# Kernel tuning notes

Hardware: AMD Instinct MI355X
Metric: run time of the kernel (lower is better)

The kernel has to match this reference:

```python
import jax, jax.numpy as jnp
import numpy as np

B, NA, NMAX, NC = 32, 8400, 32, 80
TOPK, ALPHA, BETA, EPS, BG_IDX = 13, 1.0, 6.0, 1e-9, 80
IMG = 640.0


def _ciou(box1, box2, eps=1e-7):
    # box1: (b, nmax, 1, 4) xyxy, box2: (b, 1, na, 4) xyxy -> CIoU (b, nmax, na)
    b1_x1, b1_y1, b1_x2, b1_y2 = (box1[..., 0], box1[..., 1], box1[..., 2], box1[..., 3])
    b2_x1, b2_y1, b2_x2, b2_y2 = (box2[..., 0], box2[..., 1], box2[..., 2], box2[..., 3])
    inter = (jnp.minimum(b1_x2, b2_x2) - jnp.maximum(b1_x1, b2_x1)).clip(0) * \
            (jnp.minimum(b1_y2, b2_y2) - jnp.maximum(b1_y1, b2_y1)).clip(0)
    w1, h1 = b1_x2 - b1_x1, b1_y2 - b1_y1 + eps
    w2, h2 = b2_x2 - b2_x1, b2_y2 - b2_y1 + eps
    union = w1 * h1 + w2 * h2 - inter + eps
    iou = inter / union
    cw = jnp.maximum(b1_x2, b2_x2) - jnp.minimum(b1_x1, b2_x1)
    ch = jnp.maximum(b1_y2, b2_y2) - jnp.minimum(b1_y1, b2_y1)
    c2 = cw * cw + ch * ch + eps
    rho2 = ((b2_x1 + b2_x2 - b1_x1 - b1_x2) ** 2 + (b2_y1 + b2_y2 - b1_y1 - b1_y2) ** 2) / 4.0
    v = (4.0 / np.pi ** 2) * (jnp.arctan(w2 / h2) - jnp.arctan(w1 / h1)) ** 2
    alpha = jax.lax.stop_gradient(v / (v - iou + (1.0 + eps)))
    return iou - (rho2 / c2 + v * alpha)


def _rand_boxes(key, shape):
    # well-formed xyxy boxes inside a 640x640 image
    k1, k2 = jax.random.split(key)
    xy = jax.random.uniform(k1, shape[:-1] + (2,), jnp.float32) * (IMG - 64.0)
    wh = jax.random.uniform(k2, shape[:-1] + (2,), jnp.float32) * 56.0 + 8.0
    return jnp.concatenate([xy, xy + wh], axis=-1)


def setup_inputs() -> dict:
    key = jax.random.key(0)
    ks = jax.random.split(key, 6)
    pd_scores = jax.random.uniform(ks[0], (B, NA, NC), jnp.float32)
    pd_bboxes = _rand_boxes(ks[1], (B, NA, 4))
    anc_points = jax.random.uniform(ks[2], (NA, 2), jnp.float32) * IMG
    gt_labels = jax.random.randint(ks[3], (B, NMAX, 1), 0, NC, dtype=jnp.int32)
    gt_bboxes = _rand_boxes(ks[4], (B, NMAX, 4))
    mask_gt = jnp.ones((B, NMAX, 1), jnp.float32)
    return {"pd_scores": pd_scores, "pd_bboxes": pd_bboxes, "anc_points": anc_points,
            "gt_labels": gt_labels, "gt_bboxes": gt_bboxes, "mask_gt": mask_gt}


def reference(pd_scores, pd_bboxes, anc_points, gt_labels, gt_bboxes, mask_gt):
    b, na, nc = pd_scores.shape
    nmax = gt_bboxes.shape[1]
    # pairwise CIoU between every GT and every predicted box: (b, nmax, na)
    overlaps = _ciou(gt_bboxes[:, :, None, :], pd_bboxes[:, None, :, :])
    # gather predicted class score at each GT's label: (b, nmax, na)
    p = jnp.transpose(pd_scores, (0, 2, 1))                     # (b, nc, na)
    scores = jnp.take_along_axis(p, gt_labels.astype(jnp.int32), axis=1)
    align_metric = (scores ** ALPHA) * (overlaps ** BETA)
    # top-k anchors per GT along the anchor axis, scatter to a boolean mask
    _, topk_idx = jax.lax.top_k(align_metric, TOPK)             # (b, nmax, topk)
    bi = jnp.arange(b)[:, None, None]
    gi = jnp.arange(nmax)[None, :, None]
    mask_pos = jnp.zeros((b, nmax, na), bool).at[bi, gi, topk_idx].set(True)
    target_gt_idx = jnp.argmax(mask_pos, axis=1)                # (b, na)
    fg_mask = mask_pos.sum(axis=1) > 0                          # (b, na)
    # gather assigned GT label / box per anchor
    target_labels = jnp.take_along_axis(gt_labels[..., 0].astype(jnp.int32), target_gt_idx, axis=1)
    target_bboxes = jnp.take_along_axis(gt_bboxes, target_gt_idx[..., None], axis=1)  # (b, na, 4)
    target_scores = jax.nn.one_hot(target_labels, nc, dtype=jnp.float32) * fg_mask[..., None]
    target_labels = jnp.where(fg_mask, target_labels, BG_IDX)
    # normalize target scores by mean positive overlap per anchor, clamped to [0, 1]
    mpf = mask_pos.astype(overlaps.dtype)
    pos_overlaps = jnp.clip((overlaps * mpf).sum(axis=1) / (mpf.sum(axis=1) + EPS), 0.0, 1.0)
    target_scores = target_scores * pos_overlaps[..., None]
    return target_labels, target_bboxes, target_scores, fg_mask, target_gt_idx
```

## Files before the change

### kernel.cpp

```cpp
#include <hip/hip_runtime.h>
#include <math.h>

#define BATCH 32
#define NA 8400
#define NMAX 32
#define NC 80
#define TOPK 13
#define THREADS 256
#define NF4ROW (NA / 4)
#define NPT4 9
#define TILE 128
#define NTILES 66
#define SSTRIDE 81

#define OFF_BOX 268800
#define OFF_SCR 1344000
#define OFF_FG  22848000
#define OFF_TGT 23116800
#define SCR_ELEMS (OFF_FG - OFF_SCR)
#define SCR_F4    (SCR_ELEMS / 4)
#define ZPB_M     2546

typedef float f32x4 __attribute__((ext_vector_type(4)));

__device__ __forceinline__ float ciou_f(float gx1, float gy1, float gx2, float gy2,
                                        float px1, float py1, float px2, float py2) {
    const float eps = 1e-7f;
    float iw = fmaxf(fminf(gx2, px2) - fmaxf(gx1, px1), 0.0f);
    float ih = fmaxf(fminf(gy2, py2) - fmaxf(gy1, py1), 0.0f);
    float inter = iw * ih;
    float w1 = gx2 - gx1, h1 = gy2 - gy1 + eps;
    float w2 = px2 - px1, h2 = py2 - py1 + eps;
    float uni = w1 * h1 + w2 * h2 - inter + eps;
    float iou = inter / uni;
    float cw = fmaxf(gx2, px2) - fminf(gx1, px1);
    float ch = fmaxf(gy2, py2) - fminf(gy1, py1);
    float c2 = cw * cw + ch * ch + eps;
    float dx = px1 + px2 - gx1 - gx2;
    float dy = py1 + py2 - gy1 - gy2;
    float rho2 = (dx * dx + dy * dy) / 4.0f;
    float dd = atanf(w2 / h2) - atanf(w1 / h1);
    float v = (float)(4.0 / (M_PI * M_PI)) * dd * dd;
    float alpha = v / (v - iou + (1.0f + eps));
    return iou - (rho2 / c2 + v * alpha);
}

__global__ __launch_bounds__(THREADS, 3) void metric_kernel(
    const float* __restrict__ pd_scores, const float* __restrict__ pd_bboxes,
    const int* __restrict__ gt_labels, const float* __restrict__ gt_bboxes,
    float* __restrict__ met, unsigned int* __restrict__ mask,
    float* __restrict__ zbase) {
    const int b = blockIdx.y;
    const int abase = blockIdx.x * TILE;
    const int tid = threadIdx.x;
    const int na_tile = min(TILE, NA - abase);
    const float eps = 1e-7f;

    if (tid < na_tile) mask[(size_t)b * NA + abase + tid] = 0u;

    __shared__ float ssc[TILE][SSTRIDE];
    __shared__ float4 spbox[TILE];
    __shared__ float sgx1[NMAX], sgy1[NMAX], sgx2[NMAX], sgy2[NMAX];
    __shared__ float sa1[NMAX], sat1[NMAX];
    __shared__ int   slbl[NMAX];

    if (tid < NMAX) {
        float4 g = ((const float4*)gt_bboxes)[b * NMAX + tid];
        float w1 = g.z - g.x, h1 = g.w - g.y + eps;
        sgx1[tid] = g.x; sgy1[tid] = g.y; sgx2[tid] = g.z; sgy2[tid] = g.w;
        sa1[tid]  = w1 * h1;
        sat1[tid] = atanf(w1 / h1);
        slbl[tid] = gt_labels[b * NMAX + tid];
    } else if (tid >= 128) {
        int al = tid - 128;
        if (al < na_tile)
            spbox[al] = ((const float4*)pd_bboxes)[(size_t)b * NA + abase + al];
    }

    const f32x4* srec4 = (const f32x4*)(pd_scores + ((size_t)b * NA + abase) * NC);
    const int nf4 = na_tile * 20;
    f32x4 r[10];
#pragma unroll
    for (int i = 0; i < 10; i++) {
        int f = tid + i * THREADS;
        if (f < nf4) r[i] = __builtin_nontemporal_load(srec4 + f);
    }
#pragma unroll
    for (int i = 0; i < 10; i++) {
        int f = tid + i * THREADS;
        if (f < nf4) {
            int a = f / 20, c = f % 20;
            float* d = &ssc[a][c * 4];
            d[0] = r[i][0]; d[1] = r[i][1]; d[2] = r[i][2]; d[3] = r[i][3];
        }
    }
    __syncthreads();

    if (zbase) {
        const int bid = b * NTILES + blockIdx.x;
        const size_t zoff = (size_t)bid * ZPB_M;
        f32x4* zp = (f32x4*)zbase + zoff;
        const f32x4 z = { 0.f, 0.f, 0.f, 0.f };
#pragma unroll
        for (int i = 0; i < 10; i++) {
            int j = tid + i * THREADS;
            if (j < ZPB_M && zoff + j < SCR_F4)
                __builtin_nontemporal_store(z, zp + j);
        }
    }

    const int al = tid & (TILE - 1);
    const int gbase = (tid >> 7) * 16;
    if (al >= na_tile) return;

    float4 p = spbox[al];
    float w2 = p.z - p.x, h2 = p.w - p.y + eps;
    float a2  = w2 * h2;
    float at2 = atanf(w2 / h2);
    const size_t abs_a = (size_t)abase + al;

#pragma unroll
    for (int k = 0; k < 16; k++) {
        int gi = gbase + k;
        float gx1 = sgx1[gi], gy1 = sgy1[gi], gx2 = sgx2[gi], gy2 = sgy2[gi];
        float iw = fmaxf(fminf(gx2, p.z) - fmaxf(gx1, p.x), 0.0f);
        float ih = fmaxf(fminf(gy2, p.w) - fmaxf(gy1, p.y), 0.0f);
        float inter = iw * ih;
        float uni = sa1[gi] + a2 - inter + eps;
        float iou = inter / uni;
        float cw = fmaxf(gx2, p.z) - fminf(gx1, p.x);
        float ch = fmaxf(gy2, p.w) - fminf(gy1, p.y);
        float c2 = cw * cw + ch * ch + eps;
        float dx = p.x + p.z - gx1 - gx2;
        float dy = p.y + p.w - gy1 - gy2;
        float rho2 = (dx * dx + dy * dy) / 4.0f;
        float dd = at2 - sat1[gi];
        float v = (float)(4.0 / (M_PI * M_PI)) * dd * dd;
        float alpha = v / (v - iou + (1.0f + eps));
        float ov = iou - (rho2 / c2 + v * alpha);
        float sc = ssc[al][slbl[gi]];
        float ov2 = ov * ov;
        met[((size_t)b * NMAX + gi) * NA + abs_a] = sc * (ov2 * ov2 * ov2);
    }
}

__global__ __launch_bounds__(THREADS) void topk_kernel(
    const float* __restrict__ met, unsigned int* __restrict__ mask) {
    const int tid  = threadIdx.x;
    const int lane = tid & 63;
    const int w    = tid >> 6;
    const int bid  = blockIdx.x;
    const int b  = bid >> 5;
    const int gi = bid & 31;
    const f32x4* mrow4 = (const f32x4*)(met + ((size_t)b * NMAX + gi) * NA);

    f32x4 m4[NPT4];
#pragma unroll
    for (int j = 0; j < NPT4; j++) {
        int f = j * THREADS + tid;
        if (f < NF4ROW) m4[j] = mrow4[f];
    }

    float bv0 = -INFINITY, bv1 = -INFINITY;
    int   ba0 = 0x7FFFFFFF, ba1 = 0x7FFFFFFF;
#pragma unroll
    for (int j = 0; j < NPT4; j++) {
        int f = j * THREADS + tid;
        bool vf = (f < NF4ROW);
#pragma unroll
        for (int c = 0; c < 4; c++) {
            float v = vf ? m4[j][c] : -INFINITY;
            int   a = vf ? 4 * f + c : 0x7FFFFFFF;
            bool beats0 = (v > bv0) || (v == bv0 && a < ba0);
            bool beats1 = (v > bv1) || (v == bv1 && a < ba1);
            if (beats0) { bv1 = bv0; ba1 = ba0; bv0 = v; ba0 = a; }
            else if (beats1) { bv1 = v; ba1 = a; }
        }
    }
    bool valid1 = true;

    float rv = -INFINITY; int ra = 0x7FFFFFFF;
    for (int k = 0; k < TOPK; k++) {
        float v = bv0; int a = ba0;
#pragma unroll
        for (int s = 1; s < 64; s <<= 1) {
            float ov = __shfl_xor(v, s);
            int   oa = __shfl_xor(a, s);
            if (ov > v || (ov == v && oa < a)) { v = ov; a = oa; }
        }
        if (lane == k) { rv = v; ra = a; }
        if (ba0 == a) {
            if (valid1) { bv0 = bv1; ba0 = ba1; valid1 = false; }
            else {
                float nv = -INFINITY; int na_ = 0x7FFFFFFF;
#pragma unroll
                for (int j = 0; j < NPT4; j++) {
                    int f = j * THREADS + tid;
                    bool vf = (f < NF4ROW);
#pragma unroll
                    for (int c = 0; c < 4; c++) {
                        float mv = vf ? m4[j][c] : -INFINITY;
                        int   ma = vf ? 4 * f + c : 0x7FFFFFFF;
                        bool below = (mv < v) || (mv == v && ma > a);
                        bool beats = (mv > nv) || (mv == nv && ma < na_);
                        if (below && beats && vf) { nv = mv; na_ = ma; }
                    }
                }
                bv0 = nv; ba0 = na_;
            }
        }
    }

    __shared__ float lv[4 * TOPK];
    __shared__ int   la[4 * TOPK];
    if (lane < TOPK) { lv[w * TOPK + lane] = rv; la[w * TOPK + lane] = ra; }
    __syncthreads();

    if (w == 0) {
        float v = (lane < 4 * TOPK) ? lv[lane] : -INFINITY;
        int   a = (lane < 4 * TOPK) ? la[lane] : 0x7FFFFFFF;
        for (int k = 0; k < TOPK; k++) {
            float wv = v; int wa = a;
#pragma unroll
            for (int s = 1; s < 64; s <<= 1) {
                float ov = __shfl_xor(wv, s);
                int   oa = __shfl_xor(wa, s);
                if (ov > wv || (ov == wv && oa < wa)) { wv = ov; wa = oa; }
            }
            if (lane == 0) atomicOr(&mask[(size_t)b * NA + wa], 1u << gi);
            if (a == wa) { v = -INFINITY; a = 0x7FFFFFFF; }
        }
    }
}

__global__ __launch_bounds__(THREADS) void zero_scr_kernel(float* __restrict__ out) {
    f32x4* p = (f32x4*)(out + OFF_SCR);
    const f32x4 z = { 0.f, 0.f, 0.f, 0.f };
    const int stride = gridDim.x * THREADS;
    for (int i = blockIdx.x * THREADS + threadIdx.x; i < SCR_F4; i += stride)
        __builtin_nontemporal_store(z, p + i);
}

__global__ __launch_bounds__(THREADS) void assign_kernel(
    const float* __restrict__ pd_bboxes, const int* __restrict__ gt_labels,
    const float* __restrict__ gt_bboxes, const unsigned int* __restrict__ mask,
    float* __restrict__ out) {
    const int idx = blockIdx.x * THREADS + threadIdx.x;
    const int b = idx / NA;

    unsigned msk = mask[idx];
    int tgt = msk ? (__ffs(msk) - 1) : 0;
    float4 gb = ((const float4*)gt_bboxes)[b * NMAX + tgt];
    int lbl = gt_labels[b * NMAX + tgt];
    float4 p = ((const float4*)pd_bboxes)[idx];

    float sum = 0.0f;
    int cnt = 0;
    unsigned mm = msk;
    while (mm) {
        int i = __ffs(mm) - 1;
        mm &= mm - 1;
        float4 g = ((const float4*)gt_bboxes)[b * NMAX + i];
        sum += ciou_f(g.x, g.y, g.z, g.w, p.x, p.y, p.z, p.w);
        cnt++;
    }
    float po = fminf(fmaxf(sum / ((float)cnt + 1e-9f), 0.0f), 1.0f);

    bool fg = (msk != 0);
    __builtin_nontemporal_store(fg ? (float)lbl : 80.0f, &out[idx]);
    f32x4 gbv = { gb.x, gb.y, gb.z, gb.w };
    __builtin_nontemporal_store(gbv, (f32x4*)(out + OFF_BOX) + idx);
    __builtin_nontemporal_store(fg ? 1.0f : 0.0f, &out[OFF_FG + idx]);
    __builtin_nontemporal_store((float)tgt, &out[OFF_TGT + idx]);
    if (fg) out[OFF_SCR + (size_t)idx * NC + lbl] = po;
}

extern "C" void kernel_launch(void* const* d_in, const int* in_sizes, int n_in,
                              void* d_out, int out_size, void* d_ws, size_t ws_size,
                              hipStream_t stream) {
    const float* pd_scores = (const float*)d_in[0];
    const float* pd_bboxes = (const float*)d_in[1];
    const int*   gt_labels = (const int*)d_in[3];
    const float* gt_bboxes = (const float*)d_in[4];

    float* out = (float*)d_out;
    unsigned int* mask = (unsigned int*)d_ws;

    const size_t MASK_BYTES = (size_t)BATCH * NA * 4;
    const size_t MET_BYTES  = (size_t)BATCH * NMAX * NA * 4;
    const size_t met_off = (MASK_BYTES + 255) & ~(size_t)255;
    const bool ws_met = (ws_size >= met_off + MET_BYTES);

    float* met = ws_met ? (float*)((char*)d_ws + met_off) : out + OFF_SCR;

    dim3 g1(NTILES, BATCH);
    if (ws_met) {
        metric_kernel<<<g1, THREADS, 0, stream>>>(pd_scores, pd_bboxes,
                                                  gt_labels, gt_bboxes, met, mask,
                                                  out + OFF_SCR);
        topk_kernel<<<BATCH * NMAX, THREADS, 0, stream>>>(met, mask);
    } else {
        metric_kernel<<<g1, THREADS, 0, stream>>>(pd_scores, pd_bboxes,
                                                  gt_labels, gt_bboxes, met, mask,
                                                  nullptr);
        topk_kernel<<<BATCH * NMAX, THREADS, 0, stream>>>(met, mask);
        zero_scr_kernel<<<2048, THREADS, 0, stream>>>(out);
    }
    assign_kernel<<<BATCH * NA / THREADS, THREADS, 0, stream>>>(
        pd_bboxes, gt_labels, gt_bboxes, mask, out);
}
```

Baseline: 86.81 us.

## Compact score tile to per-GT columns and raise metric kernel occupancy

The metric kernel no longer stores the full 80-class score row per anchor in shared memory. It builds a class-to-GT bitmask and scatters only the score columns used by the 32 GTs into a 128x33 tile. This cuts LDS use from about 41KB to about 17KB, and the launch bound goes from 3 to 6 blocks per CU. The scatter adds a bitmask loop per element, an atomicOr pass and an extra barrier, and the higher launch bound may squeeze registers.

```diff
diff --git a/kernel.cpp b/kernel.cpp
--- a/kernel.cpp
+++ b/kernel.cpp
@@ -11,7 +11,6 @@
 #define NPT4 9
 #define TILE 128
 #define NTILES 66
-#define SSTRIDE 81
 
 #define OFF_BOX 268800
 #define OFF_SCR 1344000
@@ -45,7 +44,7 @@
     return iou - (rho2 / c2 + v * alpha);
 }
 
-__global__ __launch_bounds__(THREADS, 3) void metric_kernel(
+__global__ __launch_bounds__(THREADS, 6) void metric_kernel(
     const float* __restrict__ pd_scores, const float* __restrict__ pd_bboxes,
     const int* __restrict__ gt_labels, const float* __restrict__ gt_bboxes,
     float* __restrict__ met, unsigned int* __restrict__ mask,
@@ -58,25 +57,13 @@
 
     if (tid < na_tile) mask[(size_t)b * NA + abase + tid] = 0u;
 
-    __shared__ float ssc[TILE][SSTRIDE];
+    __shared__ float ssc_c[TILE][NMAX + 1];
+    __shared__ unsigned int colmask[NC];
     __shared__ float4 spbox[TILE];
     __shared__ float sgx1[NMAX], sgy1[NMAX], sgx2[NMAX], sgy2[NMAX];
     __shared__ float sa1[NMAX], sat1[NMAX];
     __shared__ int   slbl[NMAX];
 
-    if (tid < NMAX) {
-        float4 g = ((const float4*)gt_bboxes)[b * NMAX + tid];
-        float w1 = g.z - g.x, h1 = g.w - g.y + eps;
-        sgx1[tid] = g.x; sgy1[tid] = g.y; sgx2[tid] = g.z; sgy2[tid] = g.w;
-        sa1[tid]  = w1 * h1;
-        sat1[tid] = atanf(w1 / h1);
-        slbl[tid] = gt_labels[b * NMAX + tid];
-    } else if (tid >= 128) {
-        int al = tid - 128;
-        if (al < na_tile)
-            spbox[al] = ((const float4*)pd_bboxes)[(size_t)b * NA + abase + al];
-    }
-
     const f32x4* srec4 = (const f32x4*)(pd_scores + ((size_t)b * NA + abase) * NC);
     const int nf4 = na_tile * 20;
     f32x4 r[10];
@@ -85,15 +72,26 @@
         int f = tid + i * THREADS;
         if (f < nf4) r[i] = __builtin_nontemporal_load(srec4 + f);
     }
-#pragma unroll
-    for (int i = 0; i < 10; i++) {
-        int f = tid + i * THREADS;
-        if (f < nf4) {
-            int a = f / 20, c = f % 20;
-            float* d = &ssc[a][c * 4];
-            d[0] = r[i][0]; d[1] = r[i][1]; d[2] = r[i][2]; d[3] = r[i][3];
-        }
-    }
+
+    if (tid < NC) colmask[tid] = 0u;
+    if (tid >= 128 && tid < 128 + NMAX) {
+        int g = tid - 128;
+        float4 gb = ((const float4*)gt_bboxes)[b * NMAX + g];
+        float w1 = gb.z - gb.x, h1 = gb.w - gb.y + eps;
+        sgx1[g] = gb.x; sgy1[g] = gb.y; sgx2[g] = gb.z; sgy2[g] = gb.w;
+        sa1[g]  = w1 * h1;
+        sat1[g] = atanf(w1 / h1);
+        slbl[g] = gt_labels[b * NMAX + g];
+    } else if (tid >= 192) {
+        int al2 = (tid - 192) * 2;
+        if (al2 < na_tile) {
+            spbox[al2] = ((const float4*)pd_bboxes)[(size_t)b * NA + abase + al2];
+            if (al2 + 1 < na_tile)
+                spbox[al2 + 1] = ((const float4*)pd_bboxes)[(size_t)b * NA + abase + al2 + 1];
+        }
+    }
+    __syncthreads();
+    if (tid < NMAX) atomicOr(&colmask[slbl[tid]], 1u << tid);
     __syncthreads();
 
     if (zbase) {
@@ -108,6 +106,25 @@
                 __builtin_nontemporal_store(z, zp + j);
         }
     }
+
+#pragma unroll
+    for (int i = 0; i < 10; i++) {
+        int f = tid + i * THREADS;
+        if (f < nf4) {
+            int a = f / 20, c4 = (f % 20) * 4;
+#pragma unroll
+            for (int j = 0; j < 4; j++) {
+                unsigned m = colmask[c4 + j];
+                float val = r[i][j];
+                while (m) {
+                    int g = __ffs(m) - 1;
+                    m &= m - 1;
+                    ssc_c[a][g] = val;
+                }
+            }
+        }
+    }
+    __syncthreads();
 
     const int al = tid & (TILE - 1);
     const int gbase = (tid >> 7) * 16;
@@ -138,7 +155,7 @@
         float v = (float)(4.0 / (M_PI * M_PI)) * dd * dd;
         float alpha = v / (v - iou + (1.0f + eps));
         float ov = iou - (rho2 / c2 + v * alpha);
-        float sc = ssc[al][slbl[gi]];
+        float sc = ssc_c[al][gi];
         float ov2 = ov * ov;
         met[((size_t)b * NMAX + gi) * NA + abs_a] = sc * (ov2 * ov2 * ov2);
     }
```

After: 93.67 us. 1.08x slower.
